# Kernel tuning notes

Measured on AMD Instinct MI355X. Metric: run time of the kernel, lower is better.

The kernel has to match this reference:

```python
import jax, jax.numpy as jnp
import numpy as np

B, S, F = 2, 2048, 2048
H, D = 16, 128  # F == H * D


def setup_inputs() -> dict:
    key = jax.random.key(0)
    k1, k2, k3 = jax.random.split(key, 3)
    x = jax.random.normal(k1, (B, S, F), dtype=jnp.float32)
    # causal attention mask, broadcast over batch and heads
    mask = jnp.tril(jnp.ones((S, S), dtype=bool))[None, None, :, :]
    init_std = 0.02
    c_attn_kernel = jax.random.normal(k2, (F, 3 * F), dtype=jnp.float32) * init_std
    c_attn_bias = jnp.zeros((3 * F,), dtype=jnp.float32)
    c_proj_kernel = jax.random.normal(k3, (F, F), dtype=jnp.float32) * init_std
    c_proj_bias = jnp.zeros((F,), dtype=jnp.float32)
    return {
        "x": x,
        "mask": mask,
        "c_attn_kernel": c_attn_kernel,
        "c_attn_bias": c_attn_bias,
        "c_proj_kernel": c_proj_kernel,
        "c_proj_bias": c_proj_bias,
    }


def reference(x, mask, c_attn_kernel, c_attn_bias, c_proj_kernel, c_proj_bias):
    dtype = x.dtype
    # fused QKV projection: [B,S,F] @ [F,3F] -> [B,S,3F]
    hidden = jnp.einsum('bsf,fe->bse', x, c_attn_kernel) + c_attn_bias
    q, k, v = jnp.split(hidden, 3, axis=-1)
    split = lambda t: t.reshape(t.shape[:-1] + (H, D))  # [B,S,H,D]
    q, k, v = split(q), split(k), split(v)
    q = q / jnp.sqrt(jnp.asarray(D, dtype))
    scores = jnp.einsum('bqhd,bkhd->bhqk', q, k)  # [B,H,S,S]
    big_neg = jnp.finfo(dtype).min
    scores = jnp.where(mask[..., :S, :S], scores, big_neg)
    weights = jax.nn.softmax(scores, axis=-1)
    z = jnp.einsum('bhqk,bkhd->bqhd', weights, v)  # [B,S,H,D]
    merged = z.reshape(z.shape[:-2] + (F,))  # [B,S,F]
    out = jnp.einsum('bsf,fe->bse', merged, c_proj_kernel) + c_proj_bias
    return out
```

## Files before the change

### kernel.cpp

```cpp
#include <hip/hip_runtime.h>
#include <hip/hip_bf16.h>
#include <stdint.h>

typedef __attribute__((ext_vector_type(8))) __bf16 bf16x8;
typedef __attribute__((ext_vector_type(4))) __bf16 bf16x4;
typedef __attribute__((ext_vector_type(4))) float f32x4;

#define DEV __device__ __forceinline__

static constexpr int S = 2048, F = 2048, H = 16, D = 128;
static constexpr int KDIM = F;
static constexpr float QSCALE = 0.08838834764831845f;

DEV void gll16(const void* g, void* l) {
  __builtin_amdgcn_global_load_lds(
      (const __attribute__((address_space(1))) void*)g,
      (__attribute__((address_space(3))) void*)l, 16, 0, 0);
}

DEV f32x4 mfma16(bf16x8 a, bf16x8 b, f32x4 c) {
  return __builtin_amdgcn_mfma_f32_16x16x32_bf16(a, b, c, 0, 0, 0);
}

extern __shared__ char smem[];

__global__ void k_cvt(const float* __restrict__ in, __bf16* __restrict__ out) {
  int i = blockIdx.x * 256 + threadIdx.x;
  float4 v = reinterpret_cast<const float4*>(in)[i];
  bf16x4 o = {(__bf16)v.x, (__bf16)v.y, (__bf16)v.z, (__bf16)v.w};
  reinterpret_cast<bf16x4*>(out)[i] = o;
}

__global__ void k_transpose(const float* __restrict__ in, __bf16* __restrict__ out,
                            int rows, int cols) {
  __shared__ float t[64][65];
  const int c0 = blockIdx.x * 64, r0 = blockIdx.y * 64;
  const int tx = threadIdx.x & 63, ty = threadIdx.x >> 6;
#pragma unroll
  for (int i = 0; i < 64; i += 4)
    t[ty + i][tx] = in[(size_t)(r0 + ty + i) * cols + c0 + tx];
  __syncthreads();
#pragma unroll
  for (int i = 0; i < 64; i += 4)
    out[(size_t)(c0 + ty + i) * rows + r0 + tx] = (__bf16)t[tx][ty + i];
}

template <int BM, int BN, int NBXL, int EPI>
__global__ __launch_bounds__(512, 1) void k_gp(
    const __bf16* __restrict__ A, const __bf16* __restrict__ Bt,
    const float* __restrict__ bias,
    __bf16* __restrict__ qo, __bf16* __restrict__ ko, __bf16* __restrict__ vo,
    float* __restrict__ fo) {
  constexpr int MF = BM / 32;
  constexpr int NF = BN / 64;
  constexpr int NLA = BM / 64;
  constexpr int NLB = BN / 64;
  constexpr int NL = NLA + NLB;
  constexpr int AOFF = BM * 128;
  constexpr int BUFSZ = (BM + BN) * 128;
  constexpr int NT = KDIM / 64;

  const int tid = threadIdx.x;
  const int lane = tid & 63, wid = tid >> 6;
  const int wm = wid >> 2, wn = wid & 3;
  const int ln = lane & 15, lm = lane >> 4;

  const int q8 = gridDim.x >> 3;
  const int lin = (blockIdx.x & 7) * q8 + (blockIdx.x >> 3);
  const int by = lin >> NBXL, bx = lin & ((1 << NBXL) - 1);
  const int mBase = by * BM, nBase = bx * BN;

  const int r0 = tid >> 3, cc = tid & 7;
  const int src0 = r0 * KDIM + ((cc ^ (r0 & 7)) << 3);
  const __bf16* Ab = A + (size_t)mBase * KDIM + src0;
  const __bf16* Bb = Bt + (size_t)nBase * KDIM + src0;
  const int dstBase = wid * 1024;

  auto stage = [&](char* buf, int t) {
    const __bf16* As = Ab + t * 64;
    const __bf16* Bs = Bb + t * 64;
#pragma unroll
    for (int j = 0; j < NLA; ++j)
      gll16(As + (size_t)j * 64 * KDIM, buf + j * 8192 + dstBase);
#pragma unroll
    for (int j = 0; j < NLB; ++j)
      gll16(Bs + (size_t)j * 64 * KDIM, buf + AOFF + j * 8192 + dstBase);
  };
  auto wait_nl = [&]() {
    if constexpr (NL == 6)       asm volatile("s_waitcnt vmcnt(6)" ::: "memory");
    else if constexpr (NL == 8)  asm volatile("s_waitcnt vmcnt(8)" ::: "memory");
    else                         asm volatile("s_waitcnt vmcnt(10)" ::: "memory");
  };

  int rA[2], rB[2];
#pragma unroll
  for (int ks = 0; ks < 2; ++ks) {
    const int slot = (ks * 4 + lm) ^ (ln & 7);
    rA[ks] = (wm * (BM / 2) + ln) * 128 + slot * 16;
    rB[ks] = AOFF + (wn * (BN / 4) + ln) * 128 + slot * 16;
  }

  f32x4 acc[MF][NF] = {};

  stage(smem, 0);
  stage(smem + BUFSZ, 1);
  wait_nl();
  __builtin_amdgcn_s_barrier();
  __builtin_amdgcn_sched_barrier(0);

  for (int t = 0; t < NT; ++t) {
    char* cb = smem + (t & 1) * BUFSZ;

    {
      bf16x8 a[MF], b[NF];
#pragma unroll
      for (int mi = 0; mi < MF; ++mi)
        a[mi] = *reinterpret_cast<const bf16x8*>(cb + rA[0] + mi * 2048);
#pragma unroll
      for (int ni = 0; ni < NF; ++ni)
        b[ni] = *reinterpret_cast<const bf16x8*>(cb + rB[0] + ni * 2048);
      asm volatile("s_waitcnt lgkmcnt(0)" ::: "memory");
      __builtin_amdgcn_sched_barrier(0);
      __builtin_amdgcn_s_setprio(1);
#pragma unroll
      for (int ni = 0; ni < NF; ++ni)
#pragma unroll
        for (int mi = 0; mi < MF; ++mi)
          acc[mi][ni] = mfma16(a[mi], b[ni], acc[mi][ni]);
      __builtin_amdgcn_s_setprio(0);
    }

    {
      bf16x8 a[MF], b[NF];
#pragma unroll
      for (int mi = 0; mi < MF; ++mi)
        a[mi] = *reinterpret_cast<const bf16x8*>(cb + rA[1] + mi * 2048);
#pragma unroll
      for (int ni = 0; ni < NF; ++ni)
        b[ni] = *reinterpret_cast<const bf16x8*>(cb + rB[1] + ni * 2048);
      asm volatile("s_waitcnt lgkmcnt(0)" ::: "memory");
      __builtin_amdgcn_sched_barrier(0);
      __builtin_amdgcn_s_barrier();
      if (t + 2 < NT) stage(cb, t + 2);
      __builtin_amdgcn_sched_barrier(0);
      __builtin_amdgcn_s_setprio(1);
#pragma unroll
      for (int ni = 0; ni < NF; ++ni)
#pragma unroll
        for (int mi = 0; mi < MF; ++mi)
          acc[mi][ni] = mfma16(a[mi], b[ni], acc[mi][ni]);
      __builtin_amdgcn_s_setprio(0);
    }

    if (t + 2 < NT) {
      wait_nl();
    } else if (t + 1 < NT) {
      asm volatile("s_waitcnt vmcnt(0)" ::: "memory");
    }
    if (t + 1 < NT) {
      __builtin_amdgcn_s_barrier();
      __builtin_amdgcn_sched_barrier(0);
    }
  }

  if (EPI == 0) {
#pragma unroll
    for (int mi = 0; mi < MF; ++mi) {
      const int grow = mBase + wm * (BM / 2) + mi * 16 + lm * 4;
      const int b = grow >> 11, s0 = grow & 2047;
#pragma unroll
      for (int ni = 0; ni < NF; ++ni) {
        const int gcol = nBase + wn * (BN / 4) + ni * 16 + ln;
        const float bv = bias[gcol];
        const int sec = gcol >> 11;
        const int h = (gcol >> 7) & 15, d = gcol & 127;
        const int bh = b * H + h;
        if (sec == 0) {
#pragma unroll
          for (int r = 0; r < 4; ++r)
            qo[((size_t)bh * S + s0 + r) * D + d] = (__bf16)((acc[mi][ni][r] + bv) * QSCALE);
        } else if (sec == 1) {
#pragma unroll
          for (int r = 0; r < 4; ++r)
            ko[((size_t)bh * S + s0 + r) * D + d] = (__bf16)(acc[mi][ni][r] + bv);
        } else {
          bf16x4 pv = {(__bf16)(acc[mi][ni][0] + bv), (__bf16)(acc[mi][ni][1] + bv),
                       (__bf16)(acc[mi][ni][2] + bv), (__bf16)(acc[mi][ni][3] + bv)};
          *reinterpret_cast<bf16x4*>(vo + ((size_t)bh * D + d) * S + s0) = pv;
        }
      }
    }
  } else {
#pragma unroll
    for (int mi = 0; mi < MF; ++mi) {
      const int grow = mBase + wm * (BM / 2) + mi * 16 + lm * 4;
#pragma unroll
      for (int ni = 0; ni < NF; ++ni) {
        const int gcol = nBase + wn * (BN / 4) + ni * 16 + ln;
        const float bv = bias[gcol];
#pragma unroll
        for (int r = 0; r < 4; ++r)
          fo[(size_t)(grow + r) * F + gcol] = acc[mi][ni][r] + bv;
      }
    }
  }
}

__global__ __launch_bounds__(256, 2) void k_attn(
    const __bf16* __restrict__ qb, const __bf16* __restrict__ kb,
    const __bf16* __restrict__ vtb, __bf16* __restrict__ zb) {
  const int lane = threadIdx.x & 63, w = threadIdx.x >> 6;
  const int lm = lane >> 4, ln = lane & 15;
  const int blk = blockIdx.x;
  const int u = blk & 255, v = blk >> 8;
  const int qt = v ? (u >> 4) : 15 - (u >> 4);
  const int bh = ((u & 15) << 1) | v;
  const int qw = qt * 128 + w * 32;

  const __bf16* qp = qb + (size_t)bh * S * D;
  const __bf16* kp = kb + (size_t)bh * S * D;
  const __bf16* vp = vtb + (size_t)bh * D * S;
  char* pw = smem + 65536 + w * 4096;

  int ksrc[4], kdst[4], vsrc[4], vdst[4];
#pragma unroll
  for (int j = 0; j < 4; ++j) {
    int c = (w * 4 + j) * 64 + lane;
    int kr = c >> 4, kps = (c & 15) ^ (kr & 7);
    ksrc[j] = kr * D + kps * 8;
    kdst[j] = (w * 4 + j) * 1024;
    int vr = c >> 3, vps = (c & 7) ^ (vr & 7);
    vsrc[j] = vr * S + vps * 8;
    vdst[j] = 16384 + (w * 4 + j) * 1024;
  }

  bf16x8 qf[2][4];
#pragma unroll
  for (int mi = 0; mi < 2; ++mi)
#pragma unroll
    for (int kf = 0; kf < 4; ++kf)
      qf[mi][kf] = *reinterpret_cast<const bf16x8*>(qp + (qw + mi * 16 + ln) * D + kf * 32 + lm * 8);

  f32x4 Oa[2][8] = {};
  float mrow[2][4], lrow[2][4];
#pragma unroll
  for (int mi = 0; mi < 2; ++mi)
#pragma unroll
    for (int r = 0; r < 4; ++r) { mrow[mi][r] = -3.0e38f; lrow[mi][r] = 0.0f; }

  const int ktEnd = 2 * qt + 1;

#pragma unroll
  for (int j = 0; j < 4; ++j) gll16(kp + ksrc[j], smem + kdst[j]);
#pragma unroll
  for (int j = 0; j < 4; ++j) gll16(vp + vsrc[j], smem + vdst[j]);
  asm volatile("s_waitcnt vmcnt(0)" ::: "memory");
  __builtin_amdgcn_s_barrier();
  __builtin_amdgcn_sched_barrier(0);

  for (int kt = 0; kt <= ktEnd; ++kt) {
    const int kv0 = kt * 64;
    const int cur = kt & 1;

    if (kt < ktEnd) {
      const int nk = (kt + 1) * 64;
      char* nbuf = smem + (cur ^ 1) * 32768;
#pragma unroll
      for (int j = 0; j < 4; ++j) gll16(kp + (size_t)nk * D + ksrc[j], nbuf + kdst[j]);
#pragma unroll
      for (int j = 0; j < 4; ++j) gll16(vp + nk + vsrc[j], nbuf + vdst[j]);
    }

    if (kv0 <= qw + 31) {
      const char* Kb = smem + cur * 32768;
      const char* Vb = Kb + 16384;
      const bool diag = (kv0 + 63 > qw);

      f32x4 sacc[2][4] = {};
#pragma unroll
      for (int kf = 0; kf < 4; ++kf) {
        bf16x8 kfr[4];
#pragma unroll
        for (int ni = 0; ni < 4; ++ni) {
          int row = ni * 16 + ln;
          int ch = (kf * 4 + lm) ^ (row & 7);
          kfr[ni] = *reinterpret_cast<const bf16x8*>(Kb + row * 256 + ch * 16);
        }
        __builtin_amdgcn_s_setprio(1);
#pragma unroll
        for (int mi = 0; mi < 2; ++mi)
#pragma unroll
          for (int ni = 0; ni < 4; ++ni)
            sacc[mi][ni] = mfma16(qf[mi][kf], kfr[ni], sacc[mi][ni]);
        __builtin_amdgcn_s_setprio(0);
      }

      if (diag) {
#pragma unroll
        for (int ni = 0; ni < 4; ++ni) {
          int c = kv0 + ni * 16 + ln;
#pragma unroll
          for (int mi = 0; mi < 2; ++mi) {
            int q0r = qw + mi * 16 + lm * 4;
#pragma unroll
            for (int r = 0; r < 4; ++r)
              if (c > q0r + r) sacc[mi][ni][r] = -1e30f;
          }
        }
      }

#pragma unroll
      for (int mi = 0; mi < 2; ++mi)
#pragma unroll
        for (int r = 0; r < 4; ++r) {
          float mx = fmaxf(fmaxf(sacc[mi][0][r], sacc[mi][1][r]),
                           fmaxf(sacc[mi][2][r], sacc[mi][3][r]));
          mx = fmaxf(mx, __shfl_xor(mx, 1, 64));
          mx = fmaxf(mx, __shfl_xor(mx, 2, 64));
          mx = fmaxf(mx, __shfl_xor(mx, 4, 64));
          mx = fmaxf(mx, __shfl_xor(mx, 8, 64));
          float mnew = fmaxf(mrow[mi][r], mx);
          float corr = __expf(mrow[mi][r] - mnew);
          mrow[mi][r] = mnew;
          float rs = 0.0f;
#pragma unroll
          for (int ni = 0; ni < 4; ++ni) {
            float p = __expf(sacc[mi][ni][r] - mnew);
            sacc[mi][ni][r] = p;
            rs += p;
          }
          lrow[mi][r] = lrow[mi][r] * corr + rs;
#pragma unroll
          for (int ni = 0; ni < 8; ++ni) Oa[mi][ni][r] *= corr;
        }

#pragma unroll
      for (int mi = 0; mi < 2; ++mi)
#pragma unroll
        for (int ni = 0; ni < 4; ++ni)
#pragma unroll
          for (int r = 0; r < 4; ++r) {
            int row = mi * 16 + lm * 4 + r;
            int bo = (row * 128 + (ni * 16 + ln) * 2) ^ ((row & 7) << 4);
            *reinterpret_cast<__bf16*>(pw + bo) = (__bf16)sacc[mi][ni][r];
          }

      asm volatile("s_waitcnt lgkmcnt(0)" ::: "memory");
      __builtin_amdgcn_sched_barrier(0);

#pragma unroll
      for (int kf = 0; kf < 2; ++kf) {
        bf16x8 pfr[2], vfr[8];
#pragma unroll
        for (int mi = 0; mi < 2; ++mi) {
          int row = mi * 16 + ln;
          int ch = (kf * 4 + lm) ^ (row & 7);
          pfr[mi] = *reinterpret_cast<const bf16x8*>(pw + row * 128 + ch * 16);
        }
#pragma unroll
        for (int ni = 0; ni < 8; ++ni) {
          int row = ni * 16 + ln;
          int ch = (kf * 4 + lm) ^ (row & 7);
          vfr[ni] = *reinterpret_cast<const bf16x8*>(Vb + row * 128 + ch * 16);
        }
        __builtin_amdgcn_s_setprio(1);
#pragma unroll
        for (int mi = 0; mi < 2; ++mi)
#pragma unroll
          for (int ni = 0; ni < 8; ++ni)
            Oa[mi][ni] = mfma16(pfr[mi], vfr[ni], Oa[mi][ni]);
        __builtin_amdgcn_s_setprio(0);
      }
    }

    asm volatile("s_waitcnt vmcnt(0) lgkmcnt(0)" ::: "memory");
    __builtin_amdgcn_s_barrier();
    __builtin_amdgcn_sched_barrier(0);
  }

#pragma unroll
  for (int mi = 0; mi < 2; ++mi)
#pragma unroll
    for (int r = 0; r < 4; ++r) {
      float ls = lrow[mi][r];
      ls += __shfl_xor(ls, 1, 64);
      ls += __shfl_xor(ls, 2, 64);
      ls += __shfl_xor(ls, 4, 64);
      ls += __shfl_xor(ls, 8, 64);
      lrow[mi][r] = 1.0f / ls;
    }
  const int b = bh >> 4, h = bh & 15;
#pragma unroll
  for (int mi = 0; mi < 2; ++mi)
#pragma unroll
    for (int ni = 0; ni < 8; ++ni) {
      int d = ni * 16 + ln;
#pragma unroll
      for (int r = 0; r < 4; ++r) {
        int qrow = qw + mi * 16 + lm * 4 + r;
        zb[(size_t)(b * S + qrow) * F + h * D + d] = (__bf16)(Oa[mi][ni][r] * lrow[mi][r]);
      }
    }
}

extern "C" void kernel_launch(void* const* d_in, const int* in_sizes, int n_in,
                              void* d_out, int out_size, void* d_ws, size_t ws_size,
                              hipStream_t stream) {
  const float* x = (const float*)d_in[0];
  const float* w_attn = (const float*)d_in[2];
  const float* b_attn = (const float*)d_in[3];
  const float* w_proj = (const float*)d_in[4];
  const float* b_proj = (const float*)d_in[5];
  float* out = (float*)d_out;

  char* ws = (char*)d_ws;
  __bf16* xb    = (__bf16*)(ws + 0);
  __bf16* wqkv  = (__bf16*)(ws + 16777216);
  __bf16* wpro  = (__bf16*)(ws + 41943040);
  __bf16* qb    = (__bf16*)(ws + 50331648);
  __bf16* kb    = (__bf16*)(ws + 67108864);
  __bf16* vtb   = (__bf16*)(ws + 83886080);
  __bf16* zb    = xb;

  (void)hipFuncSetAttribute((const void*)k_gp<128, 384, 4, 0>,
                            hipFuncAttributeMaxDynamicSharedMemorySize, 131072);
  (void)hipFuncSetAttribute((const void*)k_gp<128, 256, 3, 1>,
                            hipFuncAttributeMaxDynamicSharedMemorySize, 98304);
  (void)hipFuncSetAttribute((const void*)k_attn,
                            hipFuncAttributeMaxDynamicSharedMemorySize, 81920);

  k_cvt<<<8192, 256, 0, stream>>>(x, xb);
  k_transpose<<<dim3(96, 32), 256, 0, stream>>>(w_attn, wqkv, 2048, 6144);
  k_transpose<<<dim3(32, 32), 256, 0, stream>>>(w_proj, wpro, 2048, 2048);
  k_gp<128, 384, 4, 0><<<512, 512, 131072, stream>>>(xb, wqkv, b_attn, qb, kb, vtb, nullptr);
  k_attn<<<512, 256, 81920, stream>>>(qb, kb, vtb, zb);
  k_gp<128, 256, 3, 1><<<256, 512, 98304, stream>>>(zb, wpro, b_proj, nullptr, nullptr, nullptr, out);
}
```

Before: 257.3 us.

## Interleave LDS fragment loads with MFMA quarters in GEMM main loop

Splits each k-tile's MFMA work into four half-N quarters, issuing the next k-step's LDS fragment reads between quarters instead of waiting on all loads before each half. The aim is to hide LDS read latency behind matrix-core work and to move the barrier and next-tile global staging later in the iteration. It adds an NL==4 waitcnt case for smaller tile configs. The cost is higher register pressure from holding two fragment sets, and the compiler may reorder LDS waits without explicit sched barriers.

```diff
diff --git a/kernel.cpp b/kernel.cpp
--- a/kernel.cpp
+++ b/kernel.cpp
@@ -53,6 +53,7 @@
     float* __restrict__ fo) {
   constexpr int MF = BM / 32;
   constexpr int NF = BN / 64;
+  constexpr int NH = NF / 2;
   constexpr int NLA = BM / 64;
   constexpr int NLB = BN / 64;
   constexpr int NL = NLA + NLB;
@@ -87,7 +88,8 @@
       gll16(Bs + (size_t)j * 64 * KDIM, buf + AOFF + j * 8192 + dstBase);
   };
   auto wait_nl = [&]() {
-    if constexpr (NL == 6)       asm volatile("s_waitcnt vmcnt(6)" ::: "memory");
+    if constexpr (NL == 4)       asm volatile("s_waitcnt vmcnt(4)" ::: "memory");
+    else if constexpr (NL == 6)  asm volatile("s_waitcnt vmcnt(6)" ::: "memory");
     else if constexpr (NL == 8)  asm volatile("s_waitcnt vmcnt(8)" ::: "memory");
     else                         asm volatile("s_waitcnt vmcnt(10)" ::: "memory");
   };
@@ -110,47 +112,65 @@
 
   for (int t = 0; t < NT; ++t) {
     char* cb = smem + (t & 1) * BUFSZ;
-
-    {
-      bf16x8 a[MF], b[NF];
+    bf16x8 a0[MF], a1[MF], b0[NF], b1[NF];
+
+#pragma unroll
+    for (int mi = 0; mi < MF; ++mi)
+      a0[mi] = *reinterpret_cast<const bf16x8*>(cb + rA[0] + mi * 2048);
+#pragma unroll
+    for (int ni = 0; ni < NH; ++ni)
+      b0[ni] = *reinterpret_cast<const bf16x8*>(cb + rB[0] + ni * 2048);
+#pragma unroll
+    for (int ni = NH; ni < NF; ++ni)
+      b0[ni] = *reinterpret_cast<const bf16x8*>(cb + rB[0] + ni * 2048);
+
+    __builtin_amdgcn_s_setprio(1);
+#pragma unroll
+    for (int ni = 0; ni < NH; ++ni)
 #pragma unroll
       for (int mi = 0; mi < MF; ++mi)
-        a[mi] = *reinterpret_cast<const bf16x8*>(cb + rA[0] + mi * 2048);
-#pragma unroll
-      for (int ni = 0; ni < NF; ++ni)
-        b[ni] = *reinterpret_cast<const bf16x8*>(cb + rB[0] + ni * 2048);
-      asm volatile("s_waitcnt lgkmcnt(0)" ::: "memory");
-      __builtin_amdgcn_sched_barrier(0);
-      __builtin_amdgcn_s_setprio(1);
-#pragma unroll
-      for (int ni = 0; ni < NF; ++ni)
-#pragma unroll
-        for (int mi = 0; mi < MF; ++mi)
-          acc[mi][ni] = mfma16(a[mi], b[ni], acc[mi][ni]);
-      __builtin_amdgcn_s_setprio(0);
-    }
-
-    {
-      bf16x8 a[MF], b[NF];
+        acc[mi][ni] = mfma16(a0[mi], b0[ni], acc[mi][ni]);
+    __builtin_amdgcn_s_setprio(0);
+
+#pragma unroll
+    for (int mi = 0; mi < MF; ++mi)
+      a1[mi] = *reinterpret_cast<const bf16x8*>(cb + rA[1] + mi * 2048);
+#pragma unroll
+    for (int ni = NH; ni < NF; ++ni)
+      b1[ni] = *reinterpret_cast<const bf16x8*>(cb + rB[1] + ni * 2048);
+
+    __builtin_amdgcn_s_setprio(1);
+#pragma unroll
+    for (int ni = NH; ni < NF; ++ni)
 #pragma unroll
       for (int mi = 0; mi < MF; ++mi)
-        a[mi] = *reinterpret_cast<const bf16x8*>(cb + rA[1] + mi * 2048);
-#pragma unroll
-      for (int ni = 0; ni < NF; ++ni)
-        b[ni] = *reinterpret_cast<const bf16x8*>(cb + rB[1] + ni * 2048);
-      asm volatile("s_waitcnt lgkmcnt(0)" ::: "memory");
-      __builtin_amdgcn_sched_barrier(0);
-      __builtin_amdgcn_s_barrier();
-      if (t + 2 < NT) stage(cb, t + 2);
-      __builtin_amdgcn_sched_barrier(0);
-      __builtin_amdgcn_s_setprio(1);
-#pragma unroll
-      for (int ni = 0; ni < NF; ++ni)
-#pragma unroll
-        for (int mi = 0; mi < MF; ++mi)
-          acc[mi][ni] = mfma16(a[mi], b[ni], acc[mi][ni]);
-      __builtin_amdgcn_s_setprio(0);
-    }
+        acc[mi][ni] = mfma16(a0[mi], b0[ni], acc[mi][ni]);
+    __builtin_amdgcn_s_setprio(0);
+
+#pragma unroll
+    for (int ni = 0; ni < NH; ++ni)
+      b1[ni] = *reinterpret_cast<const bf16x8*>(cb + rB[1] + ni * 2048);
+
+    __builtin_amdgcn_s_setprio(1);
+#pragma unroll
+    for (int ni = NH; ni < NF; ++ni)
+#pragma unroll
+      for (int mi = 0; mi < MF; ++mi)
+        acc[mi][ni] = mfma16(a1[mi], b1[ni], acc[mi][ni]);
+    __builtin_amdgcn_s_setprio(0);
+
+    asm volatile("s_waitcnt lgkmcnt(0)" ::: "memory");
+    __builtin_amdgcn_s_barrier();
+    __builtin_amdgcn_sched_barrier(0);
+    if (t + 2 < NT) stage(cb, t + 2);
+
+    __builtin_amdgcn_s_setprio(1);
+#pragma unroll
+    for (int ni = 0; ni < NH; ++ni)
+#pragma unroll
+      for (int mi = 0; mi < MF; ++mi)
+        acc[mi][ni] = mfma16(a1[mi], b1[ni], acc[mi][ni]);
+    __builtin_amdgcn_s_setprio(0);
 
     if (t + 2 < NT) {
       wait_nl();
```

New measurement: 258.9 us. About the same (+0.6%).
